# Kernel tuning notes

Measured on AMD Instinct MI355X. Metric: run time of the kernel, lower is better.

Reference implementation:

```python
import jax, jax.numpy as jnp
import numpy as np

B, CIN, COUT, G, HEADS = 4, 256, 256, 8, 4
K, S, P = 7, 1, 3
H = W = 32
IN_W = CIN // G
OUT_W = COUT // G


def setup_inputs() -> dict:
    key = jax.random.key(0)
    ks = jax.random.split(key, 9)
    def n(k, shape, scale=1.0):
        return jax.random.normal(k, shape, dtype=jnp.float32) * scale
    # kaiming fan_out init for the 1x1 convs (fan_out = out channels)
    return {
        "x": n(ks[0], (B, CIN, H, W)),
        "wq": n(ks[1], (G, OUT_W * HEADS, IN_W), (2.0 / (OUT_W * HEADS)) ** 0.5),
        "bq": n(ks[2], (G, OUT_W * HEADS), 0.01),
        "wk": n(ks[3], (G, OUT_W, IN_W), (2.0 / OUT_W) ** 0.5),
        "bk": n(ks[4], (G, OUT_W), 0.01),
        "wv": n(ks[5], (G, OUT_W, IN_W), (2.0 / OUT_W) ** 0.5),
        "bv": n(ks[6], (G, OUT_W), 0.01),
        "rel_h": n(ks[7], (OUT_W // 2, 1, 1, G, K, 1)),
        "rel_w": n(ks[8], (OUT_W // 2, 1, 1, G, 1, K)),
    }


def _sparse_conv(x, w, b):
    # grouped 1x1 conv, groups stacked on last axis (matches torch.stack(dim=-1))
    # x: [B, G*I, h, w]; w: [G, O, I]; b: [G, O] -> [B, O, h, w, G]
    Bn, C, hh, ww = x.shape
    xr = x.reshape(Bn, G, C // G, hh, ww)
    out = jnp.einsum('bgihw,goi->bohwg', xr, w)
    return out + b.T[None, :, None, None, :]


def _unfold(x5, k, s):
    # x5: [B, C, Hp, Wp, G] -> [B, C, Ho, Wo, G, k, k]  (torch unfold(2).unfold(3))
    Bn, C, Hp, Wp, Gn = x5.shape
    Ho = (Hp - k) // s + 1
    Wo = (Wp - k) // s + 1
    patches = jnp.stack(
        [x5[:, :, i:i + (Ho - 1) * s + 1:s, j:j + (Wo - 1) * s + 1:s, :]
         for i in range(k) for j in range(k)], axis=-1)
    return patches.reshape(Bn, C, Ho, Wo, Gn, k, k)


def reference(x, wq, bq, wk, bk, wv, bv, rel_h, rel_w):
    xp = jnp.pad(x, ((0, 0), (0, 0), (P, P), (P, P)))
    q = _sparse_conv(x, wq, bq)    # [B, OUT_W*HEADS, H, W, G]
    k = _sparse_conv(xp, wk, bk)   # [B, OUT_W, Hp, Wp, G] (bias at padded locations, as in torch)
    v = _sparse_conv(xp, wv, bv)
    k = _unfold(k, K, S)           # [B, OUT_W, H, W, G, K, K]
    v = _unfold(v, K, S)
    kh, kw = jnp.split(k, 2, axis=1)
    k = jnp.concatenate([kh + rel_h, kw + rel_w], axis=1)
    kf = k.reshape(B, OUT_W, H, W, G * K * K)
    vf = v.reshape(B, OUT_W, H, W, G * K * K)
    q = q.reshape(B, HEADS, OUT_W, H, W, G)
    # scores: sum over channel c; softmax over flattened (group, kh, kw) window
    scores = jnp.einsum('bhcxyg,bcxym->bhxygm', q, kf)
    attn = jax.nn.softmax(scores, axis=-1)
    # weighted sum over window m and heads h (matches sum(dim=1) then sum(dim=-1))
    out = jnp.einsum('bhxygm,bcxym->bcxyg', attn, vf)   # [B, OUT_W, H, W, G]
    out = jnp.transpose(out, (0, 4, 2, 3, 1)).reshape(B, -1, H, W)  # transpose(1,-1)+reshape
    return out
```

## Files before the change

### kernel.cpp

```cpp
#include <hip/hip_runtime.h>
#include <math.h>

typedef _Float16 f16;
typedef _Float16 f16x4 __attribute__((ext_vector_type(4)));
typedef _Float16 f16x8 __attribute__((ext_vector_type(8)));
typedef __bf16 bf16x2 __attribute__((ext_vector_type(2)));
typedef __bf16 bf16x4 __attribute__((ext_vector_type(4)));
typedef __bf16 bf16x4a8 __attribute__((ext_vector_type(4), aligned(8)));
typedef short s16x4 __attribute__((ext_vector_type(4)));
typedef float f32x4 __attribute__((ext_vector_type(4)));

#define MFMA_F16(a, b, c)  __builtin_amdgcn_mfma_f32_16x16x32_f16(a, b, c, 0, 0, 0)
#define MFMA_BF16_K16(a, b, c) __builtin_amdgcn_mfma_f32_16x16x16bf16_1k(a, b, c, 0, 0, 0)

#define VSS 12160

static __device__ inline f16x8 cvt8(const float* p) {
    const float4* p4 = (const float4*)p;
    float4 u0 = p4[0], u1 = p4[1];
    f16x8 r;
    r[0] = (f16)u0.x; r[1] = (f16)u0.y; r[2] = (f16)u0.z; r[3] = (f16)u0.w;
    r[4] = (f16)u1.x; r[5] = (f16)u1.y; r[6] = (f16)u1.z; r[7] = (f16)u1.w;
    return r;
}

__global__ __launch_bounds__(256) void produce_kernel(
    const float* __restrict__ x,
    const float* __restrict__ wq, const float* __restrict__ bq,
    const float* __restrict__ wk, const float* __restrict__ bk,
    const float* __restrict__ wv, const float* __restrict__ bv,
    const float* __restrict__ rel_h, const float* __restrict__ rel_w,
    f16* __restrict__ Qb, f16* __restrict__ Kb,
    __bf16* __restrict__ V4, f16* __restrict__ relp) {
    int bid = blockIdx.x;
    int t = threadIdx.x;

    if (bid == 1216) {
        for (int idx = t; idx < 448 * 32; idx += 256) {
            int c = idx & 31, key = idx >> 5;
            int kw = key & 7, ghk = key >> 3;
            int gp = (ghk * 37) >> 8;
            int kh = ghk - gp * 7;
            float v = 0.f;
            if (kw < 7)
                v = (c < 16) ? rel_h[c * 56 + gp * 7 + kh]
                             : rel_w[(c - 16) * 56 + gp * 7 + kw];
            relp[idx] = (f16)v;
        }
        return;
    }

    int hp = bid % 38, g = (bid / 38) & 7, b = bid / 304;
    bool hin = (hp >= 3 && hp < 35);
    size_t kvbase = (size_t)(b * 8 + g);
    size_t rowp = (kvbase * 38 + hp) * 10;

    if (!hin) {
        for (int idx = t; idx < 38 * 32; idx += 256) {
            int wp = idx >> 5, c = idx & 31;
            Kb[((kvbase * 38 + hp) * 38 + wp) * 32 + c] = (f16)bk[g * 32 + c];
        }
        for (int idx = t; idx < 4 * 40 * 32; idx += 256) {
            int c = idx & 31, w = (idx >> 5) % 40, s = (idx >> 5) / 40;
            int wp = s + w;
            __bf16 val = (wp <= 37) ? (__bf16)bv[g * 32 + c] : (__bf16)0.f;
            V4[((size_t)s * VSS + rowp + (w >> 2)) * 128 + c * 4 + (w & 3)] = val;
        }
        return;
    }

    int h = hp - 3;
    __shared__ __align__(16) f16 xTl[32 * 40];

    {
        int ic = t >> 3, w = (t & 7) * 4;
        float4 xv = *(const float4*)(x + (((size_t)b * 256 + g * 32 + ic) * 32 + h) * 32 + w);
        xTl[(w + 0) * 40 + ic] = (f16)xv.x;
        xTl[(w + 1) * 40 + ic] = (f16)xv.y;
        xTl[(w + 2) * 40 + ic] = (f16)xv.z;
        xTl[(w + 3) * 40 + ic] = (f16)xv.w;
    }
    __syncthreads();

    int l15 = t & 15, quad = (t >> 4) & 3, wave = t >> 6;

    f16x8 xf0 = *(const f16x8*)(xTl + l15 * 40 + quad * 8);
    f16x8 xf1 = *(const f16x8*)(xTl + (16 + l15) * 40 + quad * 8);

#pragma unroll
    for (int i = 0; i < 2; ++i) {
        int mq = wave * 2 + i;
        f16x8 wf = cvt8(wq + ((size_t)g * 128 + mq * 16 + l15) * 32 + quad * 8);
        float4 b4 = *(const float4*)(bq + g * 128 + mq * 16 + quad * 4);
#pragma unroll
        for (int Nt = 0; Nt < 2; ++Nt) {
            f32x4 d = {0.f, 0.f, 0.f, 0.f};
            d = MFMA_F16(wf, Nt ? xf1 : xf0, d);
            f16x4 q4;
            q4[0] = (f16)(d[0] + b4.x); q4[1] = (f16)(d[1] + b4.y);
            q4[2] = (f16)(d[2] + b4.z); q4[3] = (f16)(d[3] + b4.w);
            int w = Nt * 16 + l15;
            *(f16x4*)(Qb + (size_t)((b * 32 + h) * 32 + w) * 1024 + g * 128 + mq * 16 + quad * 4) = q4;
        }
    }

    if (wave < 2) {
        f16x8 wf = cvt8(wk + ((size_t)g * 32 + wave * 16 + l15) * 32 + quad * 8);
        float4 b4 = *(const float4*)(bk + g * 32 + wave * 16 + quad * 4);
#pragma unroll
        for (int Nt = 0; Nt < 2; ++Nt) {
            f32x4 d = {0.f, 0.f, 0.f, 0.f};
            d = MFMA_F16(wf, Nt ? xf1 : xf0, d);
            f16x4 k4;
            k4[0] = (f16)(d[0] + b4.x); k4[1] = (f16)(d[1] + b4.y);
            k4[2] = (f16)(d[2] + b4.z); k4[3] = (f16)(d[3] + b4.w);
            int wp = Nt * 16 + l15 + 3;
            *(f16x4*)(Kb + ((kvbase * 38 + hp) * 38 + wp) * 32 + wave * 16 + quad * 4) = k4;
        }
    } else {
        int Nt = wave - 2;
        f16x8 wf = cvt8(wv + ((size_t)g * 32 + Nt * 16 + l15) * 32 + quad * 8);
        float bias = bv[g * 32 + Nt * 16 + l15];
        int c = Nt * 16 + l15;
#pragma unroll
        for (int Mt = 0; Mt < 2; ++Mt) {
            f32x4 d = {0.f, 0.f, 0.f, 0.f};
            d = MFMA_F16(Mt ? xf1 : xf0, wf, d);
            __bf16 v0 = (__bf16)(d[0] + bias), v1 = (__bf16)(d[1] + bias);
            __bf16 v2 = (__bf16)(d[2] + bias), v3 = (__bf16)(d[3] + bias);
            int p0 = Mt * 4 + quad;
            __bf16* P0 = V4 + ((size_t)0 * VSS + rowp + p0) * 128 + c * 4;
            __bf16* P1 = V4 + ((size_t)1 * VSS + rowp + p0) * 128 + c * 4;
            __bf16* P2 = V4 + ((size_t)2 * VSS + rowp + p0) * 128 + c * 4;
            __bf16* P3 = V4 + ((size_t)3 * VSS + rowp + p0) * 128 + c * 4;
            { bf16x4a8 q; q[0] = v0; q[1] = v1; q[2] = v2; q[3] = v3; *(bf16x4a8*)P3 = q; }
            { P2[1] = v0; bf16x2 m; m[0] = v1; m[1] = v2; *(bf16x2*)(P2 + 2) = m; P2[128] = v3; }
            { bf16x2 m; m[0] = v0; m[1] = v1; *(bf16x2*)(P1 + 2) = m;
              bf16x2 n; n[0] = v2; n[1] = v3; *(bf16x2*)(P1 + 128) = n; }
            { P0[3] = v0; bf16x2 m; m[0] = v1; m[1] = v2; *(bf16x2*)(P0 + 128) = m; P0[130] = v3; }
        }
    }

    for (int idx = t; idx < 192; idx += 256) {
        int wi = idx >> 5, c = idx & 31;
        int wp = (wi < 3) ? wi : (32 + wi);
        Kb[((kvbase * 38 + hp) * 38 + wp) * 32 + c] = (f16)bk[g * 32 + c];
    }
    for (int idx = t; idx < 4 * 6 * 32; idx += 256) {
        int c = idx & 31, wi = (idx >> 5) % 6, s = (idx >> 5) / 6;
        int wp = (wi < 3) ? wi : (32 + wi);
        if (wp >= s) {
            int w = wp - s;
            V4[((size_t)s * VSS + rowp + (w >> 2)) * 128 + c * 4 + (w & 3)] =
                (__bf16)bv[g * 32 + c];
        }
    }
    for (int idx = t; idx < 4 * 5 * 32; idx += 256) {
        int c = idx & 31, j = (idx >> 5) % 5, s = (idx >> 5) / 5;
        int w = 35 + j;
        if (s + w >= 38)
            V4[((size_t)s * VSS + rowp + (w >> 2)) * 128 + c * 4 + (w & 3)] = (__bf16)0.f;
    }
}

__global__ __launch_bounds__(128, 4) void attn_kernel(
    const f16* __restrict__ Qb, const f16* __restrict__ Kb,
    const __bf16* __restrict__ V4, const f16* __restrict__ relp,
    float* __restrict__ out) {
    int bid = blockIdx.x;
    int t = threadIdx.x;
    int wvi = t >> 6;
    int pid = (bid & 7) * 512 + (bid >> 3);
    int y = pid & 31, x = (pid >> 5) & 31, b = pid >> 10;

    __shared__ __align__(16) float accS[64 * 20];

    int lane = t & 63;
    int l15 = lane & 15, quad = lane >> 4, kwl = lane & 7, p8 = (lane >> 3) & 1;
    bool oddq = (quad & 1);

    f16x8 qf[2];
    {
        const f16* qp = Qb + (size_t)pid * 1024;
        qf[0] = *(const f16x8*)(qp + l15 * 32 + quad * 8);
        qf[1] = *(const f16x8*)(qp + (16 + l15) * 32 + quad * 8);
    }

    float fsumT[2] = {0.f, 0.f};
    f32x4 acc[2][2];
#pragma unroll
    for (int ct = 0; ct < 2; ++ct)
#pragma unroll
        for (int m = 0; m < 2; ++m) acc[ct][m] = (f32x4){0.f, 0.f, 0.f, 0.f};

    int yk = y + kwl;
    if (yk > 37) yk = 37;
    int s = y & 3;
    size_t vshift = (size_t)s * VSS;

    for (int chunk = wvi * 2; chunk < wvi * 2 + 2; ++chunk) {
        int gpr = chunk * 2 + p8;
        int gpv = chunk * 2 + (quad >> 1);
        const f16* kbp = Kb + ((((size_t)(b * 8 + gpr) * 38 + x) * 38 + yk) << 5) + quad * 8;
        const f16* rpp = relp + ((size_t)(gpr * 56 + kwl) << 5) + quad * 8;
        const __bf16* vp0 = V4 +
            ((vshift + ((size_t)(b * 8 + gpv) * 38 + x) * 10 + (y >> 2) + (quad & 1)) << 7) +
            l15 * 4;
        const __bf16* vp1 = vp0 + 64;
#pragma unroll
        for (int kh = 0; kh < 7; ++kh) {
            f16x8 kb = *(const f16x8*)kbp;  kbp += 38 * 32;
            f16x8 rp = *(const f16x8*)rpp;  rpp += 256;
            kb += rp;
            s16x4 vf0 = *(const s16x4*)vp0;  vp0 += 1280;
            s16x4 vf1 = *(const s16x4*)vp1;  vp1 += 1280;
#pragma unroll
            for (int Mt = 0; Mt < 2; ++Mt) {
                f32x4 d = {0.f, 0.f, 0.f, 0.f};
                d = MFMA_F16(kb, qf[Mt], d);
                float e0 = __expf(d[0]);
                float e1 = __expf(d[1]);
                float e2 = __expf(d[2]);
                float e3 = oddq ? 0.f : __expf(d[3]);
                fsumT[Mt] += (e0 + e1) + (e2 + e3);
                bf16x4 pb;
                pb[0] = (__bf16)e0; pb[1] = (__bf16)e1;
                pb[2] = (__bf16)e2; pb[3] = (__bf16)e3;
                s16x4 pbi = __builtin_bit_cast(s16x4, pb);
                acc[0][Mt] = MFMA_BF16_K16(vf0, pbi, acc[0][Mt]);
                acc[1][Mt] = MFMA_BF16_K16(vf1, pbi, acc[1][Mt]);
            }
        }
    }

#pragma unroll
    for (int m = 0; m < 2; ++m) {
        fsumT[m] += __shfl_xor(fsumT[m], 16);
        fsumT[m] += __shfl_xor(fsumT[m], 32);
    }

    if (wvi == 1) {
        float* sp = accS + lane * 20;
        *(f32x4*)(sp + 0)  = acc[0][0];
        *(f32x4*)(sp + 4)  = acc[0][1];
        *(f32x4*)(sp + 8)  = acc[1][0];
        *(f32x4*)(sp + 12) = acc[1][1];
        sp[16] = fsumT[0];
        sp[17] = fsumT[1];
    }
    __syncthreads();
    if (wvi == 1) return;

    {
        const float* sp = accS + lane * 20;
        acc[0][0] += *(const f32x4*)(sp + 0);
        acc[0][1] += *(const f32x4*)(sp + 4);
        acc[1][0] += *(const f32x4*)(sp + 8);
        acc[1][1] += *(const f32x4*)(sp + 12);
        fsumT[0] += sp[16];
        fsumT[1] += sp[17];
    }
    float inv[2] = {1.0f / fsumT[0], 1.0f / fsumT[1]};

#pragma unroll
    for (int Mt = 0; Mt < 2; ++Mt)
#pragma unroll
        for (int ct = 0; ct < 2; ++ct) {
            float v[4];
#pragma unroll
            for (int r = 0; r < 4; ++r) {
                v[r] = acc[ct][Mt][r] * inv[Mt];
                v[r] += __shfl_xor(v[r], 1);
                v[r] += __shfl_xor(v[r], 2);
            }
            if ((l15 & 3) == 0) {
                int g = Mt * 4 + (l15 >> 2);
                float4 o4 = {v[0], v[1], v[2], v[3]};
                *(float4*)(out + ((((size_t)(b * 8 + g) * 32 + x) * 32 + y) << 5) +
                           ct * 16 + quad * 4) = o4;
            }
        }
}

extern "C" void kernel_launch(void* const* d_in, const int* in_sizes, int n_in,
                              void* d_out, int out_size, void* d_ws, size_t ws_size,
                              hipStream_t stream) {
    const float* x     = (const float*)d_in[0];
    const float* wq    = (const float*)d_in[1];
    const float* bq    = (const float*)d_in[2];
    const float* wk    = (const float*)d_in[3];
    const float* bk    = (const float*)d_in[4];
    const float* wv    = (const float*)d_in[5];
    const float* bv    = (const float*)d_in[6];
    const float* rel_h = (const float*)d_in[7];
    const float* rel_w = (const float*)d_in[8];
    float* out = (float*)d_out;

    unsigned char* ws = (unsigned char*)d_ws;
    f16*    Qb   = (f16*)ws;
    f16*    Kb   = (f16*)(ws + 8388608);
    __bf16* V4   = (__bf16*)(ws + 8388608 + 2957312);
    f16*    relp = (f16*)(ws + 8388608 + 2957312 + 12451840);

    hipLaunchKernelGGL(produce_kernel, dim3(1217), dim3(256), 0, stream,
                       x, wq, bq, wk, bk, wv, bv, rel_h, rel_w, Qb, Kb, V4, relp);
    hipLaunchKernelGGL(attn_kernel, dim3(4096), dim3(128), 0, stream,
                       Qb, Kb, V4, relp, out);
}
```

Before: 120.1 us.

## Process two adjacent x positions per block to reuse K/V window rows

Each attention block now handles two neighbouring output rows (x0 and x0+1), loading 8 K/V window rows once and using them for both positions. rel_pos offsets are kept from the previous row so the second position adds the right rel term. The change halves the number of K/V global loads per output and halves the grid to 2048 blocks. In exchange it doubles the accumulator registers, lowers the launch-bounds occupancy hint from 4 to 3, and doubles the shared-memory reduction buffer.

```diff
diff --git a/kernel.cpp b/kernel.cpp
--- a/kernel.cpp
+++ b/kernel.cpp
@@ -163,123 +163,164 @@
     }
 }
 
-__global__ __launch_bounds__(128, 4) void attn_kernel(
+__global__ __launch_bounds__(128, 3) void attn_kernel(
     const f16* __restrict__ Qb, const f16* __restrict__ Kb,
     const __bf16* __restrict__ V4, const f16* __restrict__ relp,
     float* __restrict__ out) {
     int bid = blockIdx.x;
     int t = threadIdx.x;
     int wvi = t >> 6;
-    int pid = (bid & 7) * 512 + (bid >> 3);
-    int y = pid & 31, x = (pid >> 5) & 31, b = pid >> 10;
-
-    __shared__ __align__(16) float accS[64 * 20];
+    int pp = (bid & 7) * 256 + (bid >> 3);
+    int y = pp & 31, xp = (pp >> 5) & 15, b = pp >> 9;
+    int x0 = xp * 2;
+    int pid0 = (b * 32 + x0) * 32 + y;
+
+    __shared__ __align__(16) float accS[64 * 40];
 
     int lane = t & 63;
     int l15 = lane & 15, quad = lane >> 4, kwl = lane & 7, p8 = (lane >> 3) & 1;
     bool oddq = (quad & 1);
 
-    f16x8 qf[2];
+    f16x8 qf0[2], qf1[2];
     {
-        const f16* qp = Qb + (size_t)pid * 1024;
-        qf[0] = *(const f16x8*)(qp + l15 * 32 + quad * 8);
-        qf[1] = *(const f16x8*)(qp + (16 + l15) * 32 + quad * 8);
-    }
-
-    float fsumT[2] = {0.f, 0.f};
-    f32x4 acc[2][2];
-#pragma unroll
-    for (int ct = 0; ct < 2; ++ct)
-#pragma unroll
-        for (int m = 0; m < 2; ++m) acc[ct][m] = (f32x4){0.f, 0.f, 0.f, 0.f};
+        const f16* qp = Qb + (size_t)pid0 * 1024;
+        qf0[0] = *(const f16x8*)(qp + l15 * 32 + quad * 8);
+        qf0[1] = *(const f16x8*)(qp + (16 + l15) * 32 + quad * 8);
+        qp += 32 * 1024;
+        qf1[0] = *(const f16x8*)(qp + l15 * 32 + quad * 8);
+        qf1[1] = *(const f16x8*)(qp + (16 + l15) * 32 + quad * 8);
+    }
+
+    float fsum[2][2] = {{0.f, 0.f}, {0.f, 0.f}};
+    f32x4 acc[2][2][2];
+#pragma unroll
+    for (int p = 0; p < 2; ++p)
+#pragma unroll
+        for (int ct = 0; ct < 2; ++ct)
+#pragma unroll
+            for (int m = 0; m < 2; ++m) acc[p][ct][m] = (f32x4){0.f, 0.f, 0.f, 0.f};
 
     int yk = y + kwl;
     if (yk > 37) yk = 37;
-    int s = y & 3;
-    size_t vshift = (size_t)s * VSS;
+    size_t vshift = (size_t)(y & 3) * VSS;
 
     for (int chunk = wvi * 2; chunk < wvi * 2 + 2; ++chunk) {
         int gpr = chunk * 2 + p8;
         int gpv = chunk * 2 + (quad >> 1);
-        const f16* kbp = Kb + ((((size_t)(b * 8 + gpr) * 38 + x) * 38 + yk) << 5) + quad * 8;
+        const f16* kbp = Kb + ((((size_t)(b * 8 + gpr) * 38 + x0) * 38 + yk) << 5) + quad * 8;
         const f16* rpp = relp + ((size_t)(gpr * 56 + kwl) << 5) + quad * 8;
         const __bf16* vp0 = V4 +
-            ((vshift + ((size_t)(b * 8 + gpv) * 38 + x) * 10 + (y >> 2) + (quad & 1)) << 7) +
+            ((vshift + ((size_t)(b * 8 + gpv) * 38 + x0) * 10 + (y >> 2) + (quad & 1)) << 7) +
             l15 * 4;
         const __bf16* vp1 = vp0 + 64;
-#pragma unroll
-        for (int kh = 0; kh < 7; ++kh) {
+        f16x8 rpPrev;
+#pragma unroll
+        for (int r = 0; r < 8; ++r) {
             f16x8 kb = *(const f16x8*)kbp;  kbp += 38 * 32;
-            f16x8 rp = *(const f16x8*)rpp;  rpp += 256;
-            kb += rp;
             s16x4 vf0 = *(const s16x4*)vp0;  vp0 += 1280;
             s16x4 vf1 = *(const s16x4*)vp1;  vp1 += 1280;
-#pragma unroll
-            for (int Mt = 0; Mt < 2; ++Mt) {
-                f32x4 d = {0.f, 0.f, 0.f, 0.f};
-                d = MFMA_F16(kb, qf[Mt], d);
-                float e0 = __expf(d[0]);
-                float e1 = __expf(d[1]);
-                float e2 = __expf(d[2]);
-                float e3 = oddq ? 0.f : __expf(d[3]);
-                fsumT[Mt] += (e0 + e1) + (e2 + e3);
-                bf16x4 pb;
-                pb[0] = (__bf16)e0; pb[1] = (__bf16)e1;
-                pb[2] = (__bf16)e2; pb[3] = (__bf16)e3;
-                s16x4 pbi = __builtin_bit_cast(s16x4, pb);
-                acc[0][Mt] = MFMA_BF16_K16(vf0, pbi, acc[0][Mt]);
-                acc[1][Mt] = MFMA_BF16_K16(vf1, pbi, acc[1][Mt]);
+            if (r >= 1) {
+                f16x8 kbr = kb + rpPrev;
+#pragma unroll
+                for (int Mt = 0; Mt < 2; ++Mt) {
+                    f32x4 d = {0.f, 0.f, 0.f, 0.f};
+                    d = MFMA_F16(kbr, qf1[Mt], d);
+                    float e0 = __expf(d[0]);
+                    float e1 = __expf(d[1]);
+                    float e2 = __expf(d[2]);
+                    float e3 = oddq ? 0.f : __expf(d[3]);
+                    fsum[1][Mt] += (e0 + e1) + (e2 + e3);
+                    bf16x4 pb;
+                    pb[0] = (__bf16)e0; pb[1] = (__bf16)e1;
+                    pb[2] = (__bf16)e2; pb[3] = (__bf16)e3;
+                    s16x4 pbi = __builtin_bit_cast(s16x4, pb);
+                    acc[1][0][Mt] = MFMA_BF16_K16(vf0, pbi, acc[1][0][Mt]);
+                    acc[1][1][Mt] = MFMA_BF16_K16(vf1, pbi, acc[1][1][Mt]);
+                }
             }
-        }
-    }
-
-#pragma unroll
-    for (int m = 0; m < 2; ++m) {
-        fsumT[m] += __shfl_xor(fsumT[m], 16);
-        fsumT[m] += __shfl_xor(fsumT[m], 32);
-    }
+            if (r < 7) {
+                f16x8 rp = *(const f16x8*)rpp;  rpp += 256;
+                f16x8 kbr = kb + rp;
+#pragma unroll
+                for (int Mt = 0; Mt < 2; ++Mt) {
+                    f32x4 d = {0.f, 0.f, 0.f, 0.f};
+                    d = MFMA_F16(kbr, qf0[Mt], d);
+                    float e0 = __expf(d[0]);
+                    float e1 = __expf(d[1]);
+                    float e2 = __expf(d[2]);
+                    float e3 = oddq ? 0.f : __expf(d[3]);
+                    fsum[0][Mt] += (e0 + e1) + (e2 + e3);
+                    bf16x4 pb;
+                    pb[0] = (__bf16)e0; pb[1] = (__bf16)e1;
+                    pb[2] = (__bf16)e2; pb[3] = (__bf16)e3;
+                    s16x4 pbi = __builtin_bit_cast(s16x4, pb);
+                    acc[0][0][Mt] = MFMA_BF16_K16(vf0, pbi, acc[0][0][Mt]);
+                    acc[0][1][Mt] = MFMA_BF16_K16(vf1, pbi, acc[0][1][Mt]);
+                }
+                rpPrev = rp;
+            }
+        }
+    }
+
+#pragma unroll
+    for (int p = 0; p < 2; ++p)
+#pragma unroll
+        for (int m = 0; m < 2; ++m) {
+            fsum[p][m] += __shfl_xor(fsum[p][m], 16);
+            fsum[p][m] += __shfl_xor(fsum[p][m], 32);
+        }
 
     if (wvi == 1) {
-        float* sp = accS + lane * 20;
-        *(f32x4*)(sp + 0)  = acc[0][0];
-        *(f32x4*)(sp + 4)  = acc[0][1];
-        *(f32x4*)(sp + 8)  = acc[1][0];
-        *(f32x4*)(sp + 12) = acc[1][1];
-        sp[16] = fsumT[0];
-        sp[17] = fsumT[1];
+        float* sp = accS + lane * 40;
+#pragma unroll
+        for (int p = 0; p < 2; ++p)
+#pragma unroll
+            for (int ct = 0; ct < 2; ++ct)
+#pragma unroll
+                for (int m = 0; m < 2; ++m)
+                    *(f32x4*)(sp + (p * 4 + ct * 2 + m) * 4) = acc[p][ct][m];
+        sp[32] = fsum[0][0]; sp[33] = fsum[0][1];
+        sp[34] = fsum[1][0]; sp[35] = fsum[1][1];
     }
     __syncthreads();
     if (wvi == 1) return;
 
     {
-        const float* sp = accS + lane * 20;
-        acc[0][0] += *(const f32x4*)(sp + 0);
-        acc[0][1] += *(const f32x4*)(sp + 4);
-        acc[1][0] += *(const f32x4*)(sp + 8);
-        acc[1][1] += *(const f32x4*)(sp + 12);
-        fsumT[0] += sp[16];
-        fsumT[1] += sp[17];
-    }
-    float inv[2] = {1.0f / fsumT[0], 1.0f / fsumT[1]};
-
-#pragma unroll
-    for (int Mt = 0; Mt < 2; ++Mt)
-#pragma unroll
-        for (int ct = 0; ct < 2; ++ct) {
-            float v[4];
-#pragma unroll
-            for (int r = 0; r < 4; ++r) {
-                v[r] = acc[ct][Mt][r] * inv[Mt];
-                v[r] += __shfl_xor(v[r], 1);
-                v[r] += __shfl_xor(v[r], 2);
+        const float* sp = accS + lane * 40;
+#pragma unroll
+        for (int p = 0; p < 2; ++p)
+#pragma unroll
+            for (int ct = 0; ct < 2; ++ct)
+#pragma unroll
+                for (int m = 0; m < 2; ++m)
+                    acc[p][ct][m] += *(const f32x4*)(sp + (p * 4 + ct * 2 + m) * 4);
+        fsum[0][0] += sp[32]; fsum[0][1] += sp[33];
+        fsum[1][0] += sp[34]; fsum[1][1] += sp[35];
+    }
+
+#pragma unroll
+    for (int p = 0; p < 2; ++p) {
+        float inv[2] = {1.0f / fsum[p][0], 1.0f / fsum[p][1]};
+        int x = x0 + p;
+#pragma unroll
+        for (int Mt = 0; Mt < 2; ++Mt)
+#pragma unroll
+            for (int ct = 0; ct < 2; ++ct) {
+                float v[4];
+#pragma unroll
+                for (int r = 0; r < 4; ++r) {
+                    v[r] = acc[p][ct][Mt][r] * inv[Mt];
+                    v[r] += __shfl_xor(v[r], 1);
+                    v[r] += __shfl_xor(v[r], 2);
+                }
+                if ((l15 & 3) == 0) {
+                    int g = Mt * 4 + (l15 >> 2);
+                    float4 o4 = {v[0], v[1], v[2], v[3]};
+                    *(float4*)(out + ((((size_t)(b * 8 + g) * 32 + x) * 32 + y) << 5) +
+                               ct * 16 + quad * 4) = o4;
+                }
             }
-            if ((l15 & 3) == 0) {
-                int g = Mt * 4 + (l15 >> 2);
-                float4 o4 = {v[0], v[1], v[2], v[3]};
-                *(float4*)(out + ((((size_t)(b * 8 + g) * 32 + x) * 32 + y) << 5) +
-                           ct * 16 + quad * 4) = o4;
-            }
-        }
+    }
 }
 
 extern "C" void kernel_launch(void* const* d_in, const int* in_sizes, int n_in,
@@ -304,6 +345,6 @@
 
     hipLaunchKernelGGL(produce_kernel, dim3(1217), dim3(256), 0, stream,
                        x, wq, bq, wk, bk, wv, bv, rel_h, rel_w, Qb, Kb, V4, relp);
-    hipLaunchKernelGGL(attn_kernel, dim3(4096), dim3(128), 0, stream,
+    hipLaunchKernelGGL(attn_kernel, dim3(2048), dim3(128), 0, stream,
                        Qb, Kb, V4, relp, out);
 }
```

After: 129.7 us. 1.08x slower.
